# Performance work log

Measured on AMD Instinct MI355X. Metric: run time of the kernel, lower is better.

The kernel has to match this reference:

```python
import jax, jax.numpy as jnp
import numpy as np

P, L, E, D, NL, FF = 1024, 32, 512, 768, 6, 3072
H_PA, H_TR = 4, 8
VOCAB = 256


def layer_norm(x, w, b, eps=1e-5):
    mu = x.mean(-1, keepdims=True)
    var = ((x - mu) ** 2).mean(-1, keepdims=True)
    return (x - mu) / jnp.sqrt(var + eps) * w + b


def mha(x, wqkv, bqkv, wo, bo, nheads, key_mask=None):
    # x: [B,S,E]; torch nn.MultiheadAttention semantics (scale q by 1/sqrt(d))
    B, S, Emb = x.shape
    d = Emb // nheads
    qkv = x @ wqkv.T + bqkv
    q, k, v = jnp.split(qkv, 3, axis=-1)
    hd = lambda t: t.reshape(B, S, nheads, d).transpose(0, 2, 1, 3)
    q, k, v = hd(q) * (d ** -0.5), hd(k), hd(v)
    scores = jnp.einsum('bhqd,bhkd->bhqk', q, k)
    if key_mask is not None:
        scores = jnp.where(key_mask[:, None, None, :], scores, -1e9)
    a = jax.nn.softmax(scores, axis=-1)
    o = jnp.einsum('bhqk,bhkd->bhqd', a, v).transpose(0, 2, 1, 3).reshape(B, S, Emb)
    return o @ wo.T + bo


def setup_inputs() -> dict:
    key = jax.random.key(0)
    ks = jax.random.split(key, 32)
    n = lambda i, shape, s=0.02: (jax.random.normal(ks[i], shape, dtype=jnp.float32) * s)
    x = lambda i, shape: jax.random.normal(ks[i], shape, dtype=jnp.float32) * (1.0 / np.sqrt(shape[-1]))
    tokens = jax.random.randint(ks[0], (P, L), 0, VOCAB, dtype=jnp.int32)
    lengths = jax.random.randint(ks[1], (P,), 4, L + 1, dtype=jnp.int32)
    byte_emb = n(2, (VOCAB, E)).at[0].set(0.0)  # padding_idx=0
    inp = {
        'tokens': tokens, 'lengths': lengths,
        'byte_emb': byte_emb,
        'local_pos_emb': n(3, (L, E)),
        'patch_pos_emb': n(4, (P, D)),
        'pa_qkv_w': x(5, (3 * E, E)), 'pa_qkv_b': jnp.zeros((3 * E,), jnp.float32),
        'pa_out_w': x(6, (E, E)), 'pa_out_b': jnp.zeros((E,), jnp.float32),
        'proj_w': x(7, (D, E)), 'proj_b': jnp.zeros((D,), jnp.float32),
        'layers_qkv_w': x(8, (NL, 3 * D, D)), 'layers_qkv_b': jnp.zeros((NL, 3 * D), jnp.float32),
        'layers_out_w': x(9, (NL, D, D)), 'layers_out_b': jnp.zeros((NL, D), jnp.float32),
        'layers_ln1_w': jnp.ones((NL, D), jnp.float32), 'layers_ln1_b': jnp.zeros((NL, D), jnp.float32),
        'layers_ln2_w': jnp.ones((NL, D), jnp.float32), 'layers_ln2_b': jnp.zeros((NL, D), jnp.float32),
        'layers_ff1_w': x(10, (NL, FF, D)), 'layers_ff1_b': jnp.zeros((NL, FF), jnp.float32),
        'layers_ff2_w': x(11, (NL, D, FF)), 'layers_ff2_b': jnp.zeros((NL, D), jnp.float32),
        'ln_f_w': jnp.ones((D,), jnp.float32), 'ln_f_b': jnp.zeros((D,), jnp.float32),
    }
    return inp


def reference(tokens, lengths, byte_emb, local_pos_emb, patch_pos_emb,
              pa_qkv_w, pa_qkv_b, pa_out_w, pa_out_b, proj_w, proj_b,
              layers_qkv_w, layers_qkv_b, layers_out_w, layers_out_b,
              layers_ln1_w, layers_ln1_b, layers_ln2_w, layers_ln2_b,
              layers_ff1_w, layers_ff1_b, layers_ff2_w, layers_ff2_b,
              ln_f_w, ln_f_b):
    mask = jnp.arange(L) < lengths[:, None]  # [P,L] valid-byte mask
    # encode_patches: byte embed + local positions, zero padded slots
    emb = byte_emb[tokens] + local_pos_emb[None, :, :]  # [P,L,E]
    emb = emb * mask[..., None].astype(emb.dtype)
    # per-patch MHA over bytes (key padding mask), vectorized across patches
    attn = mha(emb, pa_qkv_w, pa_qkv_b, pa_out_w, pa_out_b, H_PA, key_mask=mask)
    cnt = mask.sum(-1, keepdims=True).astype(emb.dtype)
    patch_repr = (attn * mask[..., None].astype(emb.dtype)).sum(1) / cnt  # [P,E] masked mean
    # project to hidden and add patch-level positions
    h = patch_repr @ proj_w.T + proj_b + patch_pos_emb[:P]
    h = h[None]  # [1,P,D]
    # pre-norm transformer encoder, gelu FFN
    for i in range(NL):
        hn = layer_norm(h, layers_ln1_w[i], layers_ln1_b[i])
        h = h + mha(hn, layers_qkv_w[i], layers_qkv_b[i], layers_out_w[i], layers_out_b[i], H_TR)
        hn = layer_norm(h, layers_ln2_w[i], layers_ln2_b[i])
        ff = jax.nn.gelu(hn @ layers_ff1_w[i].T + layers_ff1_b[i], approximate=False)
        h = h + ff @ layers_ff2_w[i].T + layers_ff2_b[i]
    return layer_norm(h, ln_f_w, ln_f_b)[0]  # [P,D]
```

## Files before the change

kernel.cpp:

```cpp
#include <hip/hip_runtime.h>
#include <hip/hip_bf16.h>
#include <math.h>

typedef __hip_bfloat16 bf16;
typedef unsigned short u16;
typedef __attribute__((ext_vector_type(8))) short short8;
typedef __attribute__((ext_vector_type(4))) float f32x4;
typedef __attribute__((ext_vector_type(4))) unsigned u32x4;

#define PP 1024
#define LL 32
#define EE 512
#define DD 768
#define NLAYER 6
#define FFDIM 3072

__device__ __forceinline__ float bf2f(u16 u) { return __uint_as_float(((unsigned)u) << 16); }
__device__ __forceinline__ u16 f2b(float x) {
  unsigned u = __float_as_uint(x);
  return (u16)((u + 0x7FFFu + ((u >> 16) & 1u)) >> 16);
}

__global__ __launch_bounds__(256) void cvt4(
    const float* s0, const float* s1, const float* s2, const float* s3,
    u16* d0, u16* d1, u16* d2, u16* d3,
    int n0, int n1, int n2, int n3)
{
  int r = blockIdx.y;
  const float* s = r == 0 ? s0 : r == 1 ? s1 : r == 2 ? s2 : s3;
  u16* d        = r == 0 ? d0 : r == 1 ? d1 : r == 2 ? d2 : d3;
  int n4        = r == 0 ? n0 : r == 1 ? n1 : r == 2 ? n2 : n3;
  int i = blockIdx.x * 256 + threadIdx.x;
  if (i < n4) {
    float4 v = ((const float4*)s)[i];
    ushort4 o;
    o.x = f2b(v.x); o.y = f2b(v.y); o.z = f2b(v.z); o.w = f2b(v.w);
    ((ushort4*)d)[i] = o;
  }
}

__global__ __launch_bounds__(256) void embed_table(
    const float* __restrict__ be, const float* __restrict__ lp, bf16* __restrict__ T)
{
  int i = blockIdx.x * 256 + threadIdx.x;
  int r = i >> 6, c = (i & 63) << 3;
  int t = r >> 5, l = r & 31;
  const float* bp = be + ((long)t << 9) + c;
  const float* pp = lp + ((long)l << 9) + c;
  float4 x0 = *(const float4*)bp, x1 = *(const float4*)(bp + 4);
  float4 y0 = *(const float4*)pp, y1 = *(const float4*)(pp + 4);
  short8 o;
  o[0] = (short)f2b(x0.x + y0.x); o[1] = (short)f2b(x0.y + y0.y);
  o[2] = (short)f2b(x0.z + y0.z); o[3] = (short)f2b(x0.w + y0.w);
  o[4] = (short)f2b(x1.x + y1.x); o[5] = (short)f2b(x1.y + y1.y);
  o[6] = (short)f2b(x1.z + y1.z); o[7] = (short)f2b(x1.w + y1.w);
  *(short8*)((u16*)T + ((long)r << 9) + c) = o;
}

__global__ __launch_bounds__(256) void gemm64(
    const bf16* A, long sAb, int lda,
    const bf16* B, long sBb, int ldb,
    float* Cf, bf16* Cb, long sCb, int ldc,
    const float* bias, int biasStride,
    const float* addf,
    int M, int N, int K, int act)
{
  __shared__ u16 As[2][64][72];
  __shared__ u16 Bs[2][64][72];
  const int bz = blockIdx.z;
  const u16* Ap = (const u16*)A + (long)bz * sAb;
  const u16* Bp = (const u16*)B + (long)bz * sBb;
  const long coff = (long)bz * sCb;
  const int m0 = blockIdx.x << 6, n0 = blockIdx.y << 6;
  const int tid = threadIdx.x;
  const int wave = tid >> 6, lane = tid & 63;
  const int sr = tid >> 3;
  const int scc = (tid & 7) << 3;
  const int br0 = n0 + sr, br1 = n0 + sr + 32;
  const short8 zz = {0,0,0,0,0,0,0,0};
  f32x4 acc[4] = {{0.f,0.f,0.f,0.f},{0.f,0.f,0.f,0.f},{0.f,0.f,0.f,0.f},{0.f,0.f,0.f,0.f}};

  {
    int ch = K < 64 ? K : 64;
    bool kv = scc < ch;
    short8 a0 = zz, a1 = zz, b0 = zz, b1 = zz;
    if (kv) {
      a0 = *(const short8*)(Ap + (long)(m0 + sr) * lda + scc);
      a1 = *(const short8*)(Ap + (long)(m0 + sr + 32) * lda + scc);
      if (br0 < N) b0 = *(const short8*)(Bp + (long)br0 * ldb + scc);
      if (br1 < N) b1 = *(const short8*)(Bp + (long)br1 * ldb + scc);
    }
    *(short8*)&As[0][sr][scc] = a0;
    *(short8*)&As[0][sr + 32][scc] = a1;
    *(short8*)&Bs[0][sr][scc] = b0;
    *(short8*)&Bs[0][sr + 32][scc] = b1;
  }
  __syncthreads();

  const int arow = (wave << 4) + (lane & 15);
  const int kq = (lane >> 4) << 3;
  int buf = 0;
  for (int k0 = 0; k0 < K; k0 += 64) {
    int knext = k0 + 64;
    bool more = knext < K;
    short8 a0 = zz, a1 = zz, b0 = zz, b1 = zz;
    if (more) {
      int ch = K - knext; if (ch > 64) ch = 64;
      bool kv = scc < ch;
      if (kv) {
        a0 = *(const short8*)(Ap + (long)(m0 + sr) * lda + knext + scc);
        a1 = *(const short8*)(Ap + (long)(m0 + sr + 32) * lda + knext + scc);
        if (br0 < N) b0 = *(const short8*)(Bp + (long)br0 * ldb + knext + scc);
        if (br1 < N) b1 = *(const short8*)(Bp + (long)br1 * ldb + knext + scc);
      }
    }
    int rem = K - k0; if (rem > 64) rem = 64;
    {
      short8 af = *(const short8*)&As[buf][arow][kq];
#pragma unroll
      for (int nt = 0; nt < 4; nt++) {
        short8 bfr = *(const short8*)&Bs[buf][(nt << 4) + (lane & 15)][kq];
        acc[nt] = __builtin_amdgcn_mfma_f32_16x16x32_bf16(af, bfr, acc[nt], 0, 0, 0);
      }
    }
    if (rem > 32) {
      short8 af = *(const short8*)&As[buf][arow][32 + kq];
#pragma unroll
      for (int nt = 0; nt < 4; nt++) {
        short8 bfr = *(const short8*)&Bs[buf][(nt << 4) + (lane & 15)][32 + kq];
        acc[nt] = __builtin_amdgcn_mfma_f32_16x16x32_bf16(af, bfr, acc[nt], 0, 0, 0);
      }
    }
    if (more) {
      int nb = buf ^ 1;
      *(short8*)&As[nb][sr][scc] = a0;
      *(short8*)&As[nb][sr + 32][scc] = a1;
      *(short8*)&Bs[nb][sr][scc] = b0;
      *(short8*)&Bs[nb][sr + 32][scc] = b1;
      __syncthreads();
      buf = nb;
    }
  }

  int rbase = m0 + (wave << 4) + ((lane >> 4) << 2);
#pragma unroll
  for (int nt = 0; nt < 4; nt++) {
    int c = n0 + (nt << 4) + (lane & 15);
    if (c >= N) continue;
    float bvl = bias ? bias[bz * biasStride + c] : 0.f;
    if (act == 2 && bz != 0) bvl = 0.f;
#pragma unroll
    for (int j = 0; j < 4; j++) {
      int r = rbase + j;
      long idx = coff + (long)r * ldc + c;
      float v = acc[nt][j] + bvl;
      if (addf) v += addf[idx];
      if (act == 1) v = 0.5f * v * (1.f + erff(v * 0.70710678118654752f));
      if (Cf) Cf[idx] = v;
      if (Cb) Cb[idx] = __float2bfloat16(v);
    }
  }
}

__global__ __launch_bounds__(128) void fused_attn(
    const bf16* __restrict__ qkvt,
    const bf16* __restrict__ Vt,
    float* __restrict__ Op,
    float* __restrict__ marr,
    float* __restrict__ larr)
{
  const int h = blockIdx.y;
  const int ks = blockIdx.z;
  const int wid = threadIdx.x >> 6;
  const int lane = threadIdx.x & 63;
  const int q0 = (blockIdx.x << 5) + (wid << 4);
  const int lr = lane & 15;
  const int lq = lane >> 4;
  const int kbase = ks << 8;
  const float scale = 0.10206207261596577f;

  const u16* qp = (const u16*)qkvt;
  const u16* kp = qp + 768 + h * 96 + (lq << 3);
  const u16* vp = (const u16*)Vt + ((long)(h * 96 + lr) << 10) + (lq << 3);

  short8 qf[3];
#pragma unroll
  for (int c = 0; c < 3; c++)
    qf[c] = *(const short8*)(qp + (long)(q0 + lr) * 2304 + h * 96 + (c << 5) + (lq << 3));

  f32x4 o[6] = {{0.f,0.f,0.f,0.f},{0.f,0.f,0.f,0.f},{0.f,0.f,0.f,0.f},
                {0.f,0.f,0.f,0.f},{0.f,0.f,0.f,0.f},{0.f,0.f,0.f,0.f}};
  float m = -INFINITY, l = 0.f;

  for (int k0 = kbase; k0 < kbase + 256; k0 += 32) {
    f32x4 s0 = {0.f,0.f,0.f,0.f}, s1 = {0.f,0.f,0.f,0.f};
#pragma unroll
    for (int c = 0; c < 3; c++) {
      short8 kf0 = *(const short8*)(kp + (long)(k0 + lr) * 2304 + (c << 5));
      short8 kf1 = *(const short8*)(kp + (long)(k0 + 16 + lr) * 2304 + (c << 5));
      s0 = __builtin_amdgcn_mfma_f32_16x16x32_bf16(kf0, qf[c], s0, 0, 0, 0);
      s1 = __builtin_amdgcn_mfma_f32_16x16x32_bf16(kf1, qf[c], s1, 0, 0, 0);
    }
    float e0[4], e1[4];
    float mx = -INFINITY;
#pragma unroll
    for (int r = 0; r < 4; r++) {
      e0[r] = s0[r] * scale;
      e1[r] = s1[r] * scale;
      mx = fmaxf(mx, fmaxf(e0[r], e1[r]));
    }
    mx = fmaxf(mx, __shfl_xor(mx, 16));
    mx = fmaxf(mx, __shfl_xor(mx, 32));
    float mn = fmaxf(m, mx);
    float ts = 0.f;
#pragma unroll
    for (int r = 0; r < 4; r++) {
      e0[r] = __expf(e0[r] - mn);
      e1[r] = __expf(e1[r] - mn);
      ts += e0[r] + e1[r];
    }
    ts += __shfl_xor(ts, 16);
    ts += __shfl_xor(ts, 32);
    if (!__all(mx <= m)) {
      float f = __expf(m - mn);
      float fr[4];
#pragma unroll
      for (int r = 0; r < 4; r++) fr[r] = __shfl(f, (lq << 2) + r);
#pragma unroll
      for (int n = 0; n < 6; n++)
#pragma unroll
        for (int r = 0; r < 4; r++) o[n][r] *= fr[r];
      l *= f;
    }
    l += ts;
    m = mn;

    unsigned a01 = ((unsigned)f2b(e0[1]) << 16) | f2b(e0[0]);
    unsigned a23 = ((unsigned)f2b(e0[3]) << 16) | f2b(e0[2]);
    unsigned b01 = ((unsigned)f2b(e1[1]) << 16) | f2b(e1[0]);
    unsigned b23 = ((unsigned)f2b(e1[3]) << 16) | f2b(e1[2]);
    int sA = lr + ((lq & 1) << 5);
    int sB = sA + 16;
    unsigned qa01 = (unsigned)__shfl((int)a01, sA);
    unsigned qa23 = (unsigned)__shfl((int)a23, sA);
    unsigned qb01 = (unsigned)__shfl((int)b01, sA);
    unsigned qb23 = (unsigned)__shfl((int)b23, sA);
    unsigned ra01 = (unsigned)__shfl((int)a01, sB);
    unsigned ra23 = (unsigned)__shfl((int)a23, sB);
    unsigned rb01 = (unsigned)__shfl((int)b01, sB);
    unsigned rb23 = (unsigned)__shfl((int)b23, sB);
    bool hi = lq >= 2;
    u32x4 wv;
    wv[0] = hi ? qb01 : qa01;
    wv[1] = hi ? qb23 : qa23;
    wv[2] = hi ? rb01 : ra01;
    wv[3] = hi ? rb23 : ra23;
    short8 pa = __builtin_bit_cast(short8, wv);

#pragma unroll
    for (int n = 0; n < 6; n++) {
      short8 vf = *(const short8*)(vp + (long)(n << 4) * 1024 + k0);
      o[n] = __builtin_amdgcn_mfma_f32_16x16x32_bf16(pa, vf, o[n], 0, 0, 0);
    }
  }

  float* Opf = Op + (long)(ks * 8 + h) * 98304;
#pragma unroll
  for (int r = 0; r < 4; r++)
#pragma unroll
    for (int n = 0; n < 6; n++)
      Opf[(long)(q0 + (lq << 2) + r) * 96 + (n << 4) + lr] = o[n][r];
  if (lq == 0) {
    int idx = (ks * 8 + h) * 1024 + q0 + lr;
    marr[idx] = m;
    larr[idx] = l;
  }
}

__global__ __launch_bounds__(128) void attn_combine(
    const float* __restrict__ Op, const float* __restrict__ marr,
    const float* __restrict__ larr, bf16* __restrict__ attn)
{
  int q = blockIdx.x, h = blockIdx.y;
  int t = threadIdx.x;
  int base = h * 1024 + q;
  float m0 = marr[base], m1 = marr[8192 + base];
  float m2 = marr[16384 + base], m3 = marr[24576 + base];
  float M = fmaxf(fmaxf(m0, m1), fmaxf(m2, m3));
  float w0 = __expf(m0 - M), w1 = __expf(m1 - M);
  float w2 = __expf(m2 - M), w3 = __expf(m3 - M);
  float L = larr[base] * w0 + larr[8192 + base] * w1
          + larr[16384 + base] * w2 + larr[24576 + base] * w3;
  if (t < 96) {
    long o = (long)base * 96 + t;
    float v = Op[o] * w0 + Op[786432 + o] * w1
            + Op[1572864 + o] * w2 + Op[2359296 + o] * w3;
    ((u16*)attn)[(long)q * 768 + h * 96 + t] = f2b(v / L);
  }
}

__global__ __launch_bounds__(256) void patch_attn(
    const bf16* __restrict__ qkt,
    const int* __restrict__ tokens, const int* __restrict__ lengths,
    const float* __restrict__ byte_emb, const float* __restrict__ local_pos,
    bf16* __restrict__ Z)
{
  __shared__ float wsum[4][32];
  __shared__ int tok_s[32];
  __shared__ int cnt_s;
  int p = blockIdx.x;
  int tid = threadIdx.x;
  if (tid < 32) tok_s[tid] = tokens[p * 32 + tid];
  if (tid == 0) cnt_s = lengths[p];
  __syncthreads();
  int cnt = cnt_s;
  int h = tid >> 6, lane = tid & 63;
  const int rsel = lane & 15;
  const int ksel = (lane >> 4) << 3;
  const u16* qkb = (const u16*)qkt + h * 128;
  const long r0 = ((long)((tok_s[rsel] << 5) | rsel)) << 10;
  const long r1 = ((long)((tok_s[16 + rsel] << 5) | (16 + rsel))) << 10;

  f32x4 acc[2][2] = {{{0.f,0.f,0.f,0.f},{0.f,0.f,0.f,0.f}},
                     {{0.f,0.f,0.f,0.f},{0.f,0.f,0.f,0.f}}};
#pragma unroll
  for (int kc = 0; kc < 4; kc++) {
    int ko = kc * 32 + ksel;
    short8 a0 = *(const short8*)(qkb + r0 + ko);
    short8 a1 = *(const short8*)(qkb + r1 + ko);
    short8 b0 = *(const short8*)(qkb + r0 + 512 + ko);
    short8 b1 = *(const short8*)(qkb + r1 + 512 + ko);
    acc[0][0] = __builtin_amdgcn_mfma_f32_16x16x32_bf16(a0, b0, acc[0][0], 0, 0, 0);
    acc[0][1] = __builtin_amdgcn_mfma_f32_16x16x32_bf16(a0, b1, acc[0][1], 0, 0, 0);
    acc[1][0] = __builtin_amdgcn_mfma_f32_16x16x32_bf16(a1, b0, acc[1][0], 0, 0, 0);
    acc[1][1] = __builtin_amdgcn_mfma_f32_16x16x32_bf16(a1, b1, acc[1][1], 0, 0, 0);
  }

  const float scale = 0.088388347648318447f;
  int j0 = lane & 15, j1 = 16 + j0;
  bool v0 = j0 < cnt, v1 = j1 < cnt;
  int rowq = (lane >> 4) << 2;
  float cs0 = 0.f, cs1 = 0.f;
#pragma unroll
  for (int ti = 0; ti < 2; ti++) {
    float s0[4], s1[4], mx[4], sm[4], e0[4], e1[4];
#pragma unroll
    for (int r = 0; r < 4; r++) {
      s0[r] = acc[ti][0][r] * scale;
      s1[r] = acc[ti][1][r] * scale;
      float a = v0 ? s0[r] : -1e30f;
      float b = v1 ? s1[r] : -1e30f;
      mx[r] = fmaxf(a, b);
    }
#pragma unroll
    for (int d = 1; d < 16; d <<= 1)
#pragma unroll
      for (int r = 0; r < 4; r++) mx[r] = fmaxf(mx[r], __shfl_xor(mx[r], d));
#pragma unroll
    for (int r = 0; r < 4; r++) {
      e0[r] = v0 ? __expf(s0[r] - mx[r]) : 0.f;
      e1[r] = v1 ? __expf(s1[r] - mx[r]) : 0.f;
      sm[r] = e0[r] + e1[r];
    }
#pragma unroll
    for (int d = 1; d < 16; d <<= 1)
#pragma unroll
      for (int r = 0; r < 4; r++) sm[r] += __shfl_xor(sm[r], d);
#pragma unroll
    for (int r = 0; r < 4; r++) {
      int row = ti * 16 + rowq + r;
      if (row < cnt) {
        float inv = 1.f / sm[r];
        cs0 += e0[r] * inv;
        cs1 += e1[r] * inv;
      }
    }
  }
  cs0 += __shfl_xor(cs0, 16); cs0 += __shfl_xor(cs0, 32);
  cs1 += __shfl_xor(cs1, 16); cs1 += __shfl_xor(cs1, 32);
  if (lane < 16) {
    float invc = 1.f / (float)cnt;
    wsum[h][lane] = cs0 * invc;
    wsum[h][16 + lane] = cs1 * invc;
  }
  __syncthreads();

  for (int e = tid; e < 512; e += 256) {
    float za0 = 0.f, za1 = 0.f, za2 = 0.f, za3 = 0.f;
    for (int j = 0; j < cnt; j++) {
      float ev = byte_emb[((long)tok_s[j] << 9) + e] + local_pos[((long)j << 9) + e];
      za0 += wsum[0][j] * ev;
      za1 += wsum[1][j] * ev;
      za2 += wsum[2][j] * ev;
      za3 += wsum[3][j] * ev;
    }
    long zb = (long)p * 2048;
    Z[zb + e]        = __float2bfloat16(za0);
    Z[zb + 512 + e]  = __float2bfloat16(za1);
    Z[zb + 1024 + e] = __float2bfloat16(za2);
    Z[zb + 1536 + e] = __float2bfloat16(za3);
  }
}

__global__ __launch_bounds__(256) void ln_kernel(
    const float* __restrict__ x,
    const float* __restrict__ a0, const float* __restrict__ a1,
    const float* __restrict__ a2, const float* __restrict__ a3,
    float* __restrict__ hout,
    const float* __restrict__ w, const float* __restrict__ b,
    bf16* outb, float* outf)
{
  __shared__ float red[8];
  __shared__ float mv[2];
  int row = blockIdx.x;
  long base = (long)row * DD;
  int tid = threadIdx.x, lane = tid & 63, wave = tid >> 6;
  float vv[3];
  float s = 0.f, s2 = 0.f;
#pragma unroll
  for (int j = 0; j < 3; j++) {
    long c = base + tid + j * 256;
    float v = x[c];
    if (a0) v += a0[c];
    if (a1) v += a1[c];
    if (a2) v += a2[c];
    if (a3) v += a3[c];
    if (hout) hout[c] = v;
    vv[j] = v; s += v; s2 += v * v;
  }
  for (int o = 32; o; o >>= 1) { s += __shfl_down(s, o); s2 += __shfl_down(s2, o); }
  if (lane == 0) { red[wave] = s; red[4 + wave] = s2; }
  __syncthreads();
  if (tid == 0) {
    float ts = red[0] + red[1] + red[2] + red[3];
    float ts2 = red[4] + red[5] + red[6] + red[7];
    float mu = ts / DD;
    float var = ts2 / DD - mu * mu;
    mv[0] = mu; mv[1] = rsqrtf(var + 1e-5f);
  }
  __syncthreads();
  float mu = mv[0], rstd = mv[1];
#pragma unroll
  for (int j = 0; j < 3; j++) {
    int c = tid + j * 256;
    float v = (vv[j] - mu) * rstd * w[c] + b[c];
    if (outb) outb[base + c] = __float2bfloat16(v);
    if (outf) outf[base + c] = v;
  }
}

__global__ __launch_bounds__(256) void transpose_v(
    const bf16* __restrict__ qkv, bf16* __restrict__ Vt)
{
  __shared__ u16 tile[32][33];
  int k0 = blockIdx.x << 5;
  int d0 = blockIdx.y << 5;
  int tx = threadIdx.x & 31, ty = threadIdx.x >> 5;
  const u16* q = (const u16*)qkv;
  for (int i = ty; i < 32; i += 8)
    tile[i][tx] = q[(long)(k0 + i) * 2304 + 1536 + d0 + tx];
  __syncthreads();
  u16* vt = (u16*)Vt;
  for (int i = ty; i < 32; i += 8)
    vt[(long)(d0 + i) * 1024 + k0 + tx] = tile[tx][i];
}

extern "C" void kernel_launch(void* const* d_in, const int* in_sizes, int n_in,
                              void* d_out, int out_size, void* d_ws, size_t ws_size,
                              hipStream_t stream)
{
  const int*   tokens    = (const int*)d_in[0];
  const int*   lengths   = (const int*)d_in[1];
  const float* byte_emb  = (const float*)d_in[2];
  const float* local_pos = (const float*)d_in[3];
  const float* patch_pos = (const float*)d_in[4];
  const float* pa_qkv_w  = (const float*)d_in[5];
  const float* pa_qkv_b  = (const float*)d_in[6];
  const float* pa_out_w  = (const float*)d_in[7];
  const float* pa_out_b  = (const float*)d_in[8];
  const float* proj_w    = (const float*)d_in[9];
  const float* proj_b    = (const float*)d_in[10];
  const float* Wqkv      = (const float*)d_in[11];
  const float* Bqkv      = (const float*)d_in[12];
  const float* Wout      = (const float*)d_in[13];
  const float* Bout      = (const float*)d_in[14];
  const float* ln1w      = (const float*)d_in[15];
  const float* ln1b      = (const float*)d_in[16];
  const float* ln2w      = (const float*)d_in[17];
  const float* ln2b      = (const float*)d_in[18];
  const float* W1        = (const float*)d_in[19];
  const float* B1        = (const float*)d_in[20];
  const float* W2        = (const float*)d_in[21];
  const float* B2        = (const float*)d_in[22];
  const float* lnfw      = (const float*)d_in[23];
  const float* lnfb      = (const float*)d_in[24];

  char* ws = (char*)d_ws;
  const size_t MB = 1ull << 20;
  bf16* qkT    = (bf16*)(ws);
  bf16* qkvt   = (bf16*)(ws + 16 * MB);
  bf16* Vt     = (bf16*)(ws + 21 * MB);
  bf16* attn   = (bf16*)(ws + 23 * MB);
  bf16* ffb    = (bf16*)(ws + 25 * MB);
  float* h     = (float*)(ws + 31 * MB);
  bf16* hn     = (bf16*)(ws + 34 * MB);
  u16*  Lw     = (u16*)(ws + 36 * MB);
  bf16* embT   = (bf16*)(ws + 50 * MB);
  float* hp    = (float*)(ws + 58 * MB);
  bf16* Z      = (bf16*)(ws + 64 * MB);
  bf16* o_mean = (bf16*)(ws + 68 * MB);
  bf16* t1     = (bf16*)(ws + 69 * MB);
  u16*  P1w    = (u16*)(ws + 70 * MB);
  float* marr  = (float*)(ws + 70 * MB);
  float* larr  = (float*)(ws + 70 * MB + 131072);

  const long PSTRIDE = (long)PP * DD;

  const long oLQKV = 0;
  const long oLOUT = 1769472;
  const long oLW1  = 2359296;
  const long oLW2  = 4718592;
  const long oPAQ  = 0;
  const long oPAO  = 786432;
  const long oPRJ  = 1048576;

  cvt4<<<dim3(768, 3), 256, 0, stream>>>(
      pa_qkv_w, pa_out_w, proj_w, nullptr,
      P1w + oPAQ, P1w + oPAO, P1w + oPRJ, nullptr,
      786432 / 4, 262144 / 4, 393216 / 4, 0);
  embed_table<<<2048, 256, 0, stream>>>(byte_emb, local_pos, embT);
  gemm64<<<dim3(128, 16, 1), 256, 0, stream>>>(
      embT, 0, EE, (bf16*)(P1w + oPAQ), 0, EE, nullptr, qkT, 0, 1024,
      pa_qkv_b, 0, nullptr, 8192, 1024, EE, 0);
  patch_attn<<<PP, 256, 0, stream>>>(
      qkT, tokens, lengths, byte_emb, local_pos, Z);
  gemm64<<<dim3(16, 2, 4), 256, 0, stream>>>(
      Z, 512, 2048, (bf16*)(P1w + oPAQ + 1024L * EE), 128L * EE, EE,
      nullptr, o_mean, 128, EE, pa_qkv_b + 1024, 128, nullptr, PP, 128, EE, 0);
  gemm64<<<dim3(16, 8, 1), 256, 0, stream>>>(
      o_mean, 0, EE, (bf16*)(P1w + oPAO), 0, EE, nullptr, t1, 0, EE,
      pa_out_b, 0, nullptr, PP, EE, EE, 0);
  gemm64<<<dim3(16, 12, 1), 256, 0, stream>>>(
      t1, 0, EE, (bf16*)(P1w + oPRJ), 0, EE, h, nullptr, 0, DD,
      proj_b, 0, patch_pos, PP, DD, EE, 0);

  for (int i = 0; i < NLAYER; i++) {
    cvt4<<<dim3(2304, 4), 256, 0, stream>>>(
        Wqkv + (long)i * 2304 * DD, Wout + (long)i * DD * DD,
        W1 + (long)i * FFDIM * DD, W2 + (long)i * DD * FFDIM,
        Lw + oLQKV, Lw + oLOUT, Lw + oLW1, Lw + oLW2,
        1769472 / 4, 589824 / 4, 2359296 / 4, 2359296 / 4);
    if (i == 0)
      ln_kernel<<<PP, 256, 0, stream>>>(h, nullptr, nullptr, nullptr, nullptr,
                                        nullptr, ln1w + i * DD, ln1b + i * DD, hn, nullptr);
    else
      ln_kernel<<<PP, 256, 0, stream>>>(h, hp, hp + PSTRIDE, hp + 2 * PSTRIDE, hp + 3 * PSTRIDE,
                                        h, ln1w + i * DD, ln1b + i * DD, hn, nullptr);
    gemm64<<<dim3(16, 36, 1), 256, 0, stream>>>(
        hn, 0, DD, (bf16*)(Lw + oLQKV), 0, DD, nullptr, qkvt, 0, 2304,
        Bqkv + i * 2304, 0, nullptr, PP, 2304, DD, 0);
    transpose_v<<<dim3(32, 24), 256, 0, stream>>>(qkvt, Vt);
    fused_attn<<<dim3(32, 8, 4), 128, 0, stream>>>(qkvt, Vt, hp, marr, larr);
    attn_combine<<<dim3(1024, 8), 128, 0, stream>>>(hp, marr, larr, attn);
    gemm64<<<dim3(16, 12, 2), 256, 0, stream>>>(
        attn, 384, DD, (bf16*)(Lw + oLOUT), 384, DD, hp, nullptr, PSTRIDE, DD,
        Bout + i * DD, 0, nullptr, PP, DD, 384, 2);
    ln_kernel<<<PP, 256, 0, stream>>>(h, hp, hp + PSTRIDE, nullptr, nullptr,
                                      h, ln2w + i * DD, ln2b + i * DD, hn, nullptr);
    gemm64<<<dim3(16, 48, 1), 256, 0, stream>>>(
        hn, 0, DD, (bf16*)(Lw + oLW1), 0, DD, nullptr, ffb, 0, FFDIM,
        B1 + i * FFDIM, 0, nullptr, PP, FFDIM, DD, 1);
    gemm64<<<dim3(16, 12, 4), 256, 0, stream>>>(
        ffb, 768, FFDIM, (bf16*)(Lw + oLW2), 768, FFDIM, hp, nullptr, PSTRIDE, DD,
        B2 + i * DD, 0, nullptr, PP, DD, 768, 2);
  }
  ln_kernel<<<PP, 256, 0, stream>>>(h, hp, hp + PSTRIDE, hp + 2 * PSTRIDE, hp + 3 * PSTRIDE,
                                    nullptr, lnfw, lnfb, nullptr, (float*)d_out);
}
```

Baseline: 975.2 us.

## Add 128x64 double-buffered GEMM, fuse V transpose, batch weight conversion

```diff
diff --git a/kernel.cpp b/kernel.cpp
--- a/kernel.cpp
+++ b/kernel.cpp
@@ -158,6 +158,137 @@
       if (act == 1) v = 0.5f * v * (1.f + erff(v * 0.70710678118654752f));
       if (Cf) Cf[idx] = v;
       if (Cb) Cb[idx] = __float2bfloat16(v);
+    }
+  }
+}
+
+__global__ __launch_bounds__(256) void gemm128(
+    const bf16* A, long sAb, int lda,
+    const bf16* B, long sBb, int ldb,
+    float* Cf, bf16* Cb, long sCb, int ldc,
+    const float* bias, int biasStride,
+    const float* addf,
+    int M, int N, int K, int act,
+    bf16* Cvt)
+{
+  __shared__ u16 As[2][128][72];
+  __shared__ u16 Bs[2][64][72];
+  const int bz = blockIdx.z;
+  const u16* Ap = (const u16*)A + (long)bz * sAb;
+  const u16* Bp = (const u16*)B + (long)bz * sBb;
+  const long coff = (long)bz * sCb;
+  const int m0 = blockIdx.x << 7, n0 = blockIdx.y << 6;
+  const int tid = threadIdx.x;
+  const int wave = tid >> 6, lane = tid & 63;
+  const int sr = tid >> 3;
+  const int scc = (tid & 7) << 3;
+  const int br0 = n0 + sr, br1 = n0 + sr + 32;
+  const short8 zz = {0,0,0,0,0,0,0,0};
+  f32x4 acc0[4] = {{0.f,0.f,0.f,0.f},{0.f,0.f,0.f,0.f},{0.f,0.f,0.f,0.f},{0.f,0.f,0.f,0.f}};
+  f32x4 acc1[4] = {{0.f,0.f,0.f,0.f},{0.f,0.f,0.f,0.f},{0.f,0.f,0.f,0.f},{0.f,0.f,0.f,0.f}};
+
+  {
+    int ch = K < 64 ? K : 64;
+    bool kv = scc < ch;
+    short8 a0 = zz, a1 = zz, a2 = zz, a3 = zz, b0 = zz, b1 = zz;
+    if (kv) {
+      a0 = *(const short8*)(Ap + (long)(m0 + sr) * lda + scc);
+      a1 = *(const short8*)(Ap + (long)(m0 + sr + 32) * lda + scc);
+      a2 = *(const short8*)(Ap + (long)(m0 + sr + 64) * lda + scc);
+      a3 = *(const short8*)(Ap + (long)(m0 + sr + 96) * lda + scc);
+      if (br0 < N) b0 = *(const short8*)(Bp + (long)br0 * ldb + scc);
+      if (br1 < N) b1 = *(const short8*)(Bp + (long)br1 * ldb + scc);
+    }
+    *(short8*)&As[0][sr][scc] = a0;
+    *(short8*)&As[0][sr + 32][scc] = a1;
+    *(short8*)&As[0][sr + 64][scc] = a2;
+    *(short8*)&As[0][sr + 96][scc] = a3;
+    *(short8*)&Bs[0][sr][scc] = b0;
+    *(short8*)&Bs[0][sr + 32][scc] = b1;
+  }
+  __syncthreads();
+
+  const int fr = lane & 15;
+  const int kq = (lane >> 4) << 3;
+  const int mrow = (wave << 5) + fr;
+  int buf = 0;
+  for (int k0 = 0; k0 < K; k0 += 64) {
+    int knext = k0 + 64;
+    bool more = knext < K;
+    short8 a0 = zz, a1 = zz, a2 = zz, a3 = zz, b0 = zz, b1 = zz;
+    if (more) {
+      int ch = K - knext; if (ch > 64) ch = 64;
+      bool kv = scc < ch;
+      if (kv) {
+        a0 = *(const short8*)(Ap + (long)(m0 + sr) * lda + knext + scc);
+        a1 = *(const short8*)(Ap + (long)(m0 + sr + 32) * lda + knext + scc);
+        a2 = *(const short8*)(Ap + (long)(m0 + sr + 64) * lda + knext + scc);
+        a3 = *(const short8*)(Ap + (long)(m0 + sr + 96) * lda + knext + scc);
+        if (br0 < N) b0 = *(const short8*)(Bp + (long)br0 * ldb + knext + scc);
+        if (br1 < N) b1 = *(const short8*)(Bp + (long)br1 * ldb + knext + scc);
+      }
+    }
+    int rem = K - k0; if (rem > 64) rem = 64;
+    {
+      short8 af0 = *(const short8*)&As[buf][mrow][kq];
+      short8 af1 = *(const short8*)&As[buf][mrow + 16][kq];
+#pragma unroll
+      for (int nt = 0; nt < 4; nt++) {
+        short8 bfr = *(const short8*)&Bs[buf][(nt << 4) + fr][kq];
+        acc0[nt] = __builtin_amdgcn_mfma_f32_16x16x32_bf16(af0, bfr, acc0[nt], 0, 0, 0);
+        acc1[nt] = __builtin_amdgcn_mfma_f32_16x16x32_bf16(af1, bfr, acc1[nt], 0, 0, 0);
+      }
+    }
+    if (rem > 32) {
+      short8 af0 = *(const short8*)&As[buf][mrow][32 + kq];
+      short8 af1 = *(const short8*)&As[buf][mrow + 16][32 + kq];
+#pragma unroll
+      for (int nt = 0; nt < 4; nt++) {
+        short8 bfr = *(const short8*)&Bs[buf][(nt << 4) + fr][32 + kq];
+        acc0[nt] = __builtin_amdgcn_mfma_f32_16x16x32_bf16(af0, bfr, acc0[nt], 0, 0, 0);
+        acc1[nt] = __builtin_amdgcn_mfma_f32_16x16x32_bf16(af1, bfr, acc1[nt], 0, 0, 0);
+      }
+    }
+    if (more) {
+      int nb = buf ^ 1;
+      *(short8*)&As[nb][sr][scc] = a0;
+      *(short8*)&As[nb][sr + 32][scc] = a1;
+      *(short8*)&As[nb][sr + 64][scc] = a2;
+      *(short8*)&As[nb][sr + 96][scc] = a3;
+      *(short8*)&Bs[nb][sr][scc] = b0;
+      *(short8*)&Bs[nb][sr + 32][scc] = b1;
+      __syncthreads();
+      buf = nb;
+    }
+  }
+
+  const int rb = m0 + (wave << 5) + ((lane >> 4) << 2);
+#pragma unroll
+  for (int mi = 0; mi < 2; mi++) {
+    int rbase = rb + (mi << 4);
+#pragma unroll
+    for (int nt = 0; nt < 4; nt++) {
+      int c = n0 + (nt << 4) + fr;
+      if (c >= N) continue;
+      float bvl = bias ? bias[bz * biasStride + c] : 0.f;
+      if (act == 2 && bz != 0) bvl = 0.f;
+      float vj[4];
+#pragma unroll
+      for (int j = 0; j < 4; j++) {
+        int r = rbase + j;
+        long idx = coff + (long)r * ldc + c;
+        float v = (mi ? acc1[nt][j] : acc0[nt][j]) + bvl;
+        if (addf) v += addf[idx];
+        if (act == 1) v = 0.5f * v * (1.f + erff(v * 0.70710678118654752f));
+        if (Cf) Cf[idx] = v;
+        if (Cb) Cb[idx] = __float2bfloat16(v);
+        vj[j] = v;
+      }
+      if (Cvt && c >= 1536) {
+        ushort4 tv;
+        tv.x = f2b(vj[0]); tv.y = f2b(vj[1]); tv.z = f2b(vj[2]); tv.w = f2b(vj[3]);
+        *(ushort4*)((u16*)Cvt + ((long)(c - 1536) << 10) + rbase) = tv;
+      }
     }
   }
 }
@@ -447,22 +578,6 @@
     if (outb) outb[base + c] = __float2bfloat16(v);
     if (outf) outf[base + c] = v;
   }
-}
-
-__global__ __launch_bounds__(256) void transpose_v(
-    const bf16* __restrict__ qkv, bf16* __restrict__ Vt)
-{
-  __shared__ u16 tile[32][33];
-  int k0 = blockIdx.x << 5;
-  int d0 = blockIdx.y << 5;
-  int tx = threadIdx.x & 31, ty = threadIdx.x >> 5;
-  const u16* q = (const u16*)qkv;
-  for (int i = ty; i < 32; i += 8)
-    tile[i][tx] = q[(long)(k0 + i) * 2304 + 1536 + d0 + tx];
-  __syncthreads();
-  u16* vt = (u16*)Vt;
-  for (int i = ty; i < 32; i += 8)
-    vt[(long)(d0 + i) * 1024 + k0 + tx] = tile[tx][i];
 }
 
 extern "C" void kernel_launch(void* const* d_in, const int* in_sizes, int n_in,
@@ -504,22 +619,22 @@
   bf16* ffb    = (bf16*)(ws + 25 * MB);
   float* h     = (float*)(ws + 31 * MB);
   bf16* hn     = (bf16*)(ws + 34 * MB);
-  u16*  Lw     = (u16*)(ws + 36 * MB);
   bf16* embT   = (bf16*)(ws + 50 * MB);
   float* hp    = (float*)(ws + 58 * MB);
   bf16* Z      = (bf16*)(ws + 64 * MB);
   bf16* o_mean = (bf16*)(ws + 68 * MB);
   bf16* t1     = (bf16*)(ws + 69 * MB);
   u16*  P1w    = (u16*)(ws + 70 * MB);
-  float* marr  = (float*)(ws + 70 * MB);
-  float* larr  = (float*)(ws + 70 * MB + 131072);
+  float* marr  = (float*)(ws + 74 * MB);
+  float* larr  = (float*)(ws + 74 * MB + 131072);
+  u16*  Lw6    = (u16*)(ws + 104 * MB);
 
   const long PSTRIDE = (long)PP * DD;
 
-  const long oLQKV = 0;
-  const long oLOUT = 1769472;
-  const long oLW1  = 2359296;
-  const long oLW2  = 4718592;
+  const long oQ6   = 0;
+  const long oO6   = 10616832;
+  const long oW1_6 = oO6 + 3538944;
+  const long oW2_6 = oW1_6 + 14155776;
   const long oPAQ  = 0;
   const long oPAO  = 786432;
   const long oPRJ  = 1048576;
@@ -529,9 +644,9 @@
       P1w + oPAQ, P1w + oPAO, P1w + oPRJ, nullptr,
       786432 / 4, 262144 / 4, 393216 / 4, 0);
   embed_table<<<2048, 256, 0, stream>>>(byte_emb, local_pos, embT);
-  gemm64<<<dim3(128, 16, 1), 256, 0, stream>>>(
+  gemm128<<<dim3(64, 16, 1), 256, 0, stream>>>(
       embT, 0, EE, (bf16*)(P1w + oPAQ), 0, EE, nullptr, qkT, 0, 1024,
-      pa_qkv_b, 0, nullptr, 8192, 1024, EE, 0);
+      pa_qkv_b, 0, nullptr, 8192, 1024, EE, 0, nullptr);
   patch_attn<<<PP, 256, 0, stream>>>(
       qkT, tokens, lengths, byte_emb, local_pos, Z);
   gemm64<<<dim3(16, 2, 4), 256, 0, stream>>>(
@@ -544,35 +659,38 @@
       t1, 0, EE, (bf16*)(P1w + oPRJ), 0, EE, h, nullptr, 0, DD,
       proj_b, 0, patch_pos, PP, DD, EE, 0);
 
+  cvt4<<<dim3(13824, 4), 256, 0, stream>>>(
+      Wqkv, Wout, W1, W2,
+      Lw6 + oQ6, Lw6 + oO6, Lw6 + oW1_6, Lw6 + oW2_6,
+      10616832 / 4, 3538944 / 4, 14155776 / 4, 14155776 / 4);
+
   for (int i = 0; i < NLAYER; i++) {
-    cvt4<<<dim3(2304, 4), 256, 0, stream>>>(
-        Wqkv + (long)i * 2304 * DD, Wout + (long)i * DD * DD,
-        W1 + (long)i * FFDIM * DD, W2 + (long)i * DD * FFDIM,
-        Lw + oLQKV, Lw + oLOUT, Lw + oLW1, Lw + oLW2,
-        1769472 / 4, 589824 / 4, 2359296 / 4, 2359296 / 4);
+    const bf16* LQ = (const bf16*)(Lw6 + oQ6   + (long)i * 1769472);
+    const bf16* LO = (const bf16*)(Lw6 + oO6   + (long)i * 589824);
+    const bf16* L1 = (const bf16*)(Lw6 + oW1_6 + (long)i * 2359296);
+    const bf16* L2 = (const bf16*)(Lw6 + oW2_6 + (long)i * 2359296);
     if (i == 0)
       ln_kernel<<<PP, 256, 0, stream>>>(h, nullptr, nullptr, nullptr, nullptr,
                                         nullptr, ln1w + i * DD, ln1b + i * DD, hn, nullptr);
     else
       ln_kernel<<<PP, 256, 0, stream>>>(h, hp, hp + PSTRIDE, hp + 2 * PSTRIDE, hp + 3 * PSTRIDE,
                                         h, ln1w + i * DD, ln1b + i * DD, hn, nullptr);
-    gemm64<<<dim3(16, 36, 1), 256, 0, stream>>>(
-        hn, 0, DD, (bf16*)(Lw + oLQKV), 0, DD, nullptr, qkvt, 0, 2304,
-        Bqkv + i * 2304, 0, nullptr, PP, 2304, DD, 0);
-    transpose_v<<<dim3(32, 24), 256, 0, stream>>>(qkvt, Vt);
+    gemm128<<<dim3(8, 36, 1), 256, 0, stream>>>(
+        hn, 0, DD, LQ, 0, DD, nullptr, qkvt, 0, 2304,
+        Bqkv + i * 2304, 0, nullptr, PP, 2304, DD, 0, Vt);
     fused_attn<<<dim3(32, 8, 4), 128, 0, stream>>>(qkvt, Vt, hp, marr, larr);
     attn_combine<<<dim3(1024, 8), 128, 0, stream>>>(hp, marr, larr, attn);
-    gemm64<<<dim3(16, 12, 2), 256, 0, stream>>>(
-        attn, 384, DD, (bf16*)(Lw + oLOUT), 384, DD, hp, nullptr, PSTRIDE, DD,
-        Bout + i * DD, 0, nullptr, PP, DD, 384, 2);
-    ln_kernel<<<PP, 256, 0, stream>>>(h, hp, hp + PSTRIDE, nullptr, nullptr,
+    gemm128<<<dim3(8, 12, 4), 256, 0, stream>>>(
+        attn, 192, DD, LO, 192, DD, hp, nullptr, PSTRIDE, DD,
+        Bout + i * DD, 0, nullptr, PP, DD, 192, 2, nullptr);
+    ln_kernel<<<PP, 256, 0, stream>>>(h, hp, hp + PSTRIDE, hp + 2 * PSTRIDE, hp + 3 * PSTRIDE,
                                       h, ln2w + i * DD, ln2b + i * DD, hn, nullptr);
-    gemm64<<<dim3(16, 48, 1), 256, 0, stream>>>(
-        hn, 0, DD, (bf16*)(Lw + oLW1), 0, DD, nullptr, ffb, 0, FFDIM,
-        B1 + i * FFDIM, 0, nullptr, PP, FFDIM, DD, 1);
-    gemm64<<<dim3(16, 12, 4), 256, 0, stream>>>(
-        ffb, 768, FFDIM, (bf16*)(Lw + oLW2), 768, FFDIM, hp, nullptr, PSTRIDE, DD,
-        B2 + i * DD, 0, nullptr, PP, DD, 768, 2);
+    gemm128<<<dim3(8, 48, 1), 256, 0, stream>>>(
+        hn, 0, DD, L1, 0, DD, nullptr, ffb, 0, FFDIM,
+        B1 + i * FFDIM, 0, nullptr, PP, FFDIM, DD, 1, nullptr);
+    gemm128<<<dim3(8, 12, 4), 256, 0, stream>>>(
+        ffb, 768, FFDIM, L2, 768, FFDIM, hp, nullptr, PSTRIDE, DD,
+        B2 + i * DD, 0, nullptr, PP, DD, 768, 2, nullptr);
   }
   ln_kernel<<<PP, 256, 0, stream>>>(h, hp, hp + PSTRIDE, hp + 2 * PSTRIDE, hp + 3 * PSTRIDE,
                                     nullptr, lnfw, lnfb, nullptr, (float*)d_out);
```

After: 1.044 ms. 1.07x slower.
